# Optimization experiments

Measured on AMD Instinct MI355X. Metric: run time of the kernel, lower is better.

The kernel has to match this reference:

```python
import jax, jax.numpy as jnp
import numpy as np

COMPRESS_RATIO = 4
HEAD_DIM = 512
COFF = 2  # overlap (compress_ratio == 4) doubles the projection width
EPS = 1e-6


def setup_inputs() -> dict:
    key = jax.random.key(0)
    k1, k2, k3, k4 = jax.random.split(key, 4)
    B, S, D = 4, 4096, 4096
    OD = COFF * HEAD_DIM  # 1024
    scale = 1.0 / np.sqrt(D)
    return {
        "x": jax.random.normal(k1, (B, S, D), dtype=jnp.float32),
        "wkv_w": jax.random.normal(k2, (OD, D), dtype=jnp.float32) * scale,
        "wgate_w": jax.random.normal(k3, (OD, D), dtype=jnp.float32) * scale,
        "ape": jax.random.normal(k4, (COMPRESS_RATIO, OD), dtype=jnp.float32) * 0.02,
        "norm_w": jnp.ones((HEAD_DIM,), dtype=jnp.float32),
    }


def reference(x, wkv_w, wgate_w, ape, norm_w):
    # x: [B, S, D]; windowed KV compression (NSA-style):
    # gated projection -> per-position learned abs pos embed -> window pool -> RMSNorm
    B, S, D = x.shape
    r = COMPRESS_RATIO
    nW = S // r
    kv = jnp.einsum("bsd,od->bso", x, wkv_w)          # [B, S, coff*hd]
    gate = jax.nn.sigmoid(jnp.einsum("bsd,od->bso", x, wgate_w))
    kv = kv * gate
    # add learned absolute position embedding per position-within-window
    kv = kv + jnp.tile(ape, (nW, 1))                    # [S, coff*hd] broadcast over B
    # pool each window of r tokens; split overlap streams into separate tokens
    kv = kv.reshape(B, nW, r, COFF, HEAD_DIM).mean(axis=2)  # [B, nW, coff, hd]
    kv = kv.reshape(B, nW * COFF, HEAD_DIM)                 # [B, 2*nW, hd]
    # RMSNorm over head_dim
    var = jnp.mean(kv * kv, axis=-1, keepdims=True)
    return norm_w * kv * jax.lax.rsqrt(var + EPS)
```

## Files before the change

### kernel.cpp

```cpp
#include <hip/hip_runtime.h>
#include <hip/hip_bf16.h>

#define D_DIM 4096
#define OD    1024
#define M_TOT 16384
#define N_TOT 2048
#define BM 256
#define BN 256
#define BK 64

#define GLOBAL_AS __attribute__((address_space(1)))
#define LDS_AS    __attribute__((address_space(3)))

typedef __attribute__((ext_vector_type(8))) short          bf16x8;
typedef __attribute__((ext_vector_type(8))) unsigned short u16x8;
typedef __attribute__((ext_vector_type(4))) float          f32x4;

__device__ __forceinline__ unsigned short f2bf(float f) {
    unsigned int u = __float_as_uint(f);
    u = (u + 0x7fffu + ((u >> 16) & 1u)) >> 16;
    return (unsigned short)u;
}

__device__ __forceinline__ float sigm(float x) {
    return 1.0f / (1.0f + __expf(-x));
}

__device__ __forceinline__ void gload16(const void* g, void* l) {
    __builtin_amdgcn_global_load_lds((const GLOBAL_AS void*)g, (LDS_AS void*)l, 16, 0, 0);
}

__global__ void prep_weights(const float* __restrict__ wkv,
                             const float* __restrict__ wgate,
                             unsigned short* __restrict__ Wc) {
    int t  = blockIdx.x * 256 + threadIdx.x;
    int n  = t >> 9;
    int k8 = t & 511;
    const float* src = (n & 1) ? wgate : wkv;
    const float4* s4 = (const float4*)(src + (size_t)(n >> 1) * D_DIM + k8 * 8);
    float4 a = s4[0], b = s4[1];
    u16x8 o;
    o[0] = f2bf(a.x); o[1] = f2bf(a.y); o[2] = f2bf(a.z); o[3] = f2bf(a.w);
    o[4] = f2bf(b.x); o[5] = f2bf(b.y); o[6] = f2bf(b.z); o[7] = f2bf(b.w);
    *(u16x8*)(Wc + (size_t)n * D_DIM + k8 * 8) = o;
}

__global__ void prep_x(const float* __restrict__ x, unsigned short* __restrict__ xb) {
    size_t t = (size_t)blockIdx.x * 256 + threadIdx.x;
    const float4* s = (const float4*)(x + t * 8);
    float4 a = s[0], b = s[1];
    u16x8 o;
    o[0] = f2bf(a.x); o[1] = f2bf(a.y); o[2] = f2bf(a.z); o[3] = f2bf(a.w);
    o[4] = f2bf(b.x); o[5] = f2bf(b.y); o[6] = f2bf(b.z); o[7] = f2bf(b.w);
    *(u16x8*)(xb + t * 8) = o;
}

__global__ void prep_ape(const float* __restrict__ ape, float* __restrict__ am) {
    int t = blockIdx.x * 256 + threadIdx.x;
    if (t < OD)
        am[t] = 0.25f * (ape[t] + ape[OD + t] + ape[2 * OD + t] + ape[3 * OD + t]);
}

extern __shared__ __align__(16) unsigned short smem_u16[];

__global__ __launch_bounds__(512, 2)
void gemm_fused_8ph(const unsigned short* __restrict__ A,
                    const unsigned short* __restrict__ Wc,
                    const float* __restrict__ ape_mean,
                    float* __restrict__ out_pooled) {
    unsigned short* Asb[2] = {smem_u16,               smem_u16 + BM * BK};
    unsigned short* Bsb[2] = {smem_u16 + 2 * BM * BK, smem_u16 + 3 * BM * BK};

    const int tid  = threadIdx.x;
    const int lane = tid & 63;
    const int wave = tid >> 6;
    const int wm   = wave >> 2;
    const int wn   = wave & 3;
    const int h    = lane & 15;
    const int q    = lane >> 4;

    const int bid = blockIdx.x;
    const int j   = bid >> 3;
    const int m0  = ((bid & 7) * 8 + (j >> 3)) * BM;
    const int n0  = (j & 7) * BN;

    const int sc8 = (lane & 7) ^ ((lane >> 3) & 7);
    const unsigned short* Ag = A  + (size_t)(m0 + wave * 8 + (lane >> 3)) * D_DIM + sc8 * 8;
    const unsigned short* Bg = Wc + (size_t)(n0 + (wave & 3) * 8 + (lane >> 3)) * D_DIM + sc8 * 8;
    const int bstripe = wave >> 2;

#define STAGE_A(buf, half, kofs)                                                   \
    do {                                                                           \
        gload16(Ag + (size_t)((half) * 64) * D_DIM + (kofs),                       \
                Asb[buf] + ((half) * 64 + wave * 8) * BK);                         \
        gload16(Ag + (size_t)((half) * 64 + 128) * D_DIM + (kofs),                 \
                Asb[buf] + ((half) * 64 + 128 + wave * 8) * BK);                   \
    } while (0)

#define STAGE_B(buf, qb, kofs)                                                     \
    do {                                                                           \
        const int r0_ = (qb) * 32 + bstripe * 64;                                  \
        const int r1_ = (qb) * 32 + (2 + bstripe) * 64;                            \
        gload16(Bg + (size_t)r0_ * D_DIM + (kofs),                                 \
                Bsb[buf] + (r0_ + (wave & 3) * 8) * BK);                           \
        gload16(Bg + (size_t)r1_ * D_DIM + (kofs),                                 \
                Bsb[buf] + (r1_ + (wave & 3) * 8) * BK);                           \
    } while (0)

#define LOAD_A(buf, qa, dst)                                                       \
    do {                                                                           \
        _Pragma("unroll")                                                          \
        for (int mi = 0; mi < 4; ++mi) {                                           \
            const int row = wm * 128 + ((qa) * 4 + mi) * 16 + h;                   \
            _Pragma("unroll")                                                      \
            for (int ks = 0; ks < 2; ++ks)                                         \
                dst[mi][ks] = *(const bf16x8*)&Asb[buf][(row * BK + ks * 32 +      \
                              q * 8) ^ ((row & 7) << 3)];                          \
        }                                                                          \
    } while (0)

#define LOAD_B(buf, qb, dst)                                                       \
    do {                                                                           \
        _Pragma("unroll")                                                          \
        for (int ni = 0; ni < 2; ++ni) {                                           \
            const int rw = wn * 64 + ((qb) * 2 + ni) * 16 + h;                     \
            _Pragma("unroll")                                                      \
            for (int ks = 0; ks < 2; ++ks)                                         \
                dst[ni][ks] = *(const bf16x8*)&Bsb[buf][(rw * BK + ks * 32 +       \
                              q * 8) ^ ((rw & 7) << 3)];                           \
        }                                                                          \
    } while (0)

#define MFMA_Q(qa, qb, asrc, bsrc)                                                 \
    do {                                                                           \
        __builtin_amdgcn_s_setprio(1);                                             \
        _Pragma("unroll")                                                          \
        for (int mi = 0; mi < 4; ++mi)                                             \
            _Pragma("unroll")                                                      \
            for (int ni = 0; ni < 2; ++ni)                                         \
                _Pragma("unroll")                                                  \
                for (int ks = 0; ks < 2; ++ks)                                     \
                    acc[(qa) * 4 + mi][(qb) * 2 + ni] =                            \
                        __builtin_amdgcn_mfma_f32_16x16x32_bf16(                   \
                            asrc[mi][ks], bsrc[ni][ks],                            \
                            acc[(qa) * 4 + mi][(qb) * 2 + ni], 0, 0, 0);           \
        __builtin_amdgcn_s_setprio(0);                                             \
    } while (0)

#define BAR() __builtin_amdgcn_s_barrier()
#define VMW() asm volatile("s_waitcnt vmcnt(4)" ::: "memory")

    f32x4 acc[8][4];
    const f32x4 z = {0.f, 0.f, 0.f, 0.f};
#pragma unroll
    for (int i = 0; i < 8; ++i)
#pragma unroll
        for (int jj = 0; jj < 4; ++jj) acc[i][jj] = z;

    STAGE_A(0, 0, 0); STAGE_A(0, 1, 0); STAGE_B(0, 0, 0); STAGE_B(0, 1, 0);
    STAGE_B(1, 0, 64); STAGE_A(1, 0, 64);
    VMW();
    BAR();

    for (int kt2 = 0; kt2 < D_DIM; kt2 += 2 * BK) {
        const int kb1 = kt2 + BK;
        const int kna = (kt2 + 2 * BK) & 4095;
        const int knb = (kt2 + 3 * BK) & 4095;
        bf16x8 a_reg[4][2], b0r[2][2], b1r[2][2];

        LOAD_A(0, 0, a_reg); LOAD_B(0, 0, b0r);
        STAGE_A(1, 1, kb1);
        BAR(); MFMA_Q(0, 0, a_reg, b0r); BAR();
        LOAD_B(0, 1, b1r);
        STAGE_B(1, 1, kb1);
        BAR(); MFMA_Q(0, 1, a_reg, b1r); BAR();
        LOAD_A(0, 1, a_reg);
        STAGE_B(0, 0, kna);
        BAR(); MFMA_Q(1, 1, a_reg, b1r); BAR();
        STAGE_A(0, 0, kna);
        VMW();
        BAR(); MFMA_Q(1, 0, a_reg, b0r); BAR();

        LOAD_A(1, 0, a_reg); LOAD_B(1, 0, b0r);
        STAGE_A(0, 1, kna);
        BAR(); MFMA_Q(0, 0, a_reg, b0r); BAR();
        LOAD_B(1, 1, b1r);
        STAGE_B(0, 1, kna);
        BAR(); MFMA_Q(0, 1, a_reg, b1r); BAR();
        LOAD_A(1, 1, a_reg);
        STAGE_B(1, 0, knb);
        BAR(); MFMA_Q(1, 1, a_reg, b1r); BAR();
        STAGE_A(1, 0, knb);
        VMW();
        BAR(); MFMA_Q(1, 0, a_reg, b0r); BAR();
    }
#undef STAGE_A
#undef STAGE_B
#undef LOAD_A
#undef LOAD_B
#undef MFMA_Q
#undef BAR
#undef VMW

    const bool is_kv = ((h & 1) == 0);
#pragma unroll
    for (int mi = 0; mi < 8; ++mi) {
        const int mbase = m0 + wm * 128 + mi * 16 + q * 4;
        const int wglob = mbase >> 2;
#pragma unroll
        for (int ni = 0; ni < 4; ++ni) {
            f32x4 kv = acc[mi][ni];
            float g0 = __shfl_xor(kv[0], 1);
            float g1 = __shfl_xor(kv[1], 1);
            float g2 = __shfl_xor(kv[2], 1);
            float g3 = __shfl_xor(kv[3], 1);
            if (is_kv) {
                float s = kv[0] * sigm(g0) + kv[1] * sigm(g1) +
                          kv[2] * sigm(g2) + kv[3] * sigm(g3);
                int n = n0 + wn * 64 + ni * 16 + h;
                int o = n >> 1;
                out_pooled[(size_t)wglob * OD + o] = 0.25f * s + ape_mean[o];
            }
        }
    }
}

__global__ __launch_bounds__(256)
void gemm_fused_f32(const float* __restrict__ Aptr,
                    const unsigned short* __restrict__ Wc,
                    const float* __restrict__ ape_mean,
                    float* __restrict__ out_pooled) {
    __shared__ __align__(16) unsigned short As[128 * BK];
    __shared__ __align__(16) unsigned short Bs[128 * BK];
    const int tid  = threadIdx.x;
    const int lane = tid & 63;
    const int wave = tid >> 6;
    const int wr   = wave >> 1;
    const int wc   = wave & 1;
    const int n0   = blockIdx.x * 128;
    const int m0   = blockIdx.y * 128;
    const int h    = lane & 15;
    const int q    = lane >> 4;

    f32x4 acc[4][4];
    const f32x4 z = {0.f, 0.f, 0.f, 0.f};
#pragma unroll
    for (int i = 0; i < 4; ++i)
#pragma unroll
        for (int jj = 0; jj < 4; ++jj) acc[i][jj] = z;

    for (int kt = 0; kt < D_DIM; kt += BK) {
#pragma unroll
        for (int i = 0; i < 4; ++i) {
            int chunk = tid + i * 256;
            int row = chunk >> 3, c8 = chunk & 7;
            int dst = (row * BK + c8 * 8) ^ ((row & 7) << 3);
            const float4* s = (const float4*)(Aptr + (size_t)(m0 + row) * D_DIM + kt + c8 * 8);
            float4 a = s[0], b = s[1];
            u16x8 o;
            o[0] = f2bf(a.x); o[1] = f2bf(a.y); o[2] = f2bf(a.z); o[3] = f2bf(a.w);
            o[4] = f2bf(b.x); o[5] = f2bf(b.y); o[6] = f2bf(b.z); o[7] = f2bf(b.w);
            *(u16x8*)&As[dst] = o;
        }
#pragma unroll
        for (int i = 0; i < 4; ++i) {
            int chunk = tid + i * 256;
            int row = chunk >> 3, c8 = chunk & 7;
            int dst = (row * BK + c8 * 8) ^ ((row & 7) << 3);
            *(u16x8*)&Bs[dst] =
                *(const u16x8*)(Wc + (size_t)(n0 + row) * D_DIM + kt + c8 * 8);
        }
        __syncthreads();
#pragma unroll
        for (int ks = 0; ks < 2; ++ks) {
            const int kb = ks * 32 + q * 8;
            bf16x8 af[4], bfr[4];
#pragma unroll
            for (int am = 0; am < 4; ++am) {
                int row = wr * 64 + am * 16 + h;
                af[am] = *(const bf16x8*)&As[(row * BK + kb) ^ ((row & 7) << 3)];
            }
#pragma unroll
            for (int bn = 0; bn < 4; ++bn) {
                int row = wc * 64 + bn * 16 + h;
                bfr[bn] = *(const bf16x8*)&Bs[(row * BK + kb) ^ ((row & 7) << 3)];
            }
#pragma unroll
            for (int am = 0; am < 4; ++am)
#pragma unroll
                for (int bn = 0; bn < 4; ++bn)
                    acc[am][bn] = __builtin_amdgcn_mfma_f32_16x16x32_bf16(
                        af[am], bfr[bn], acc[am][bn], 0, 0, 0);
        }
        __syncthreads();
    }
    const bool is_kv = ((h & 1) == 0);
#pragma unroll
    for (int am = 0; am < 4; ++am) {
        const int mbase = m0 + wr * 64 + am * 16 + q * 4;
        const int wglob = mbase >> 2;
#pragma unroll
        for (int bn = 0; bn < 4; ++bn) {
            f32x4 kv = acc[am][bn];
            float g0 = __shfl_xor(kv[0], 1);
            float g1 = __shfl_xor(kv[1], 1);
            float g2 = __shfl_xor(kv[2], 1);
            float g3 = __shfl_xor(kv[3], 1);
            if (is_kv) {
                float s = kv[0] * sigm(g0) + kv[1] * sigm(g1) +
                          kv[2] * sigm(g2) + kv[3] * sigm(g3);
                int n = n0 + wc * 64 + bn * 16 + h;
                int o = n >> 1;
                out_pooled[(size_t)wglob * OD + o] = 0.25f * s + ape_mean[o];
            }
        }
    }
}

__global__ void rmsnorm_inplace(float* __restrict__ out, const float* __restrict__ nw) {
    int token = blockIdx.x * 4 + (threadIdx.x >> 6);
    int lane  = threadIdx.x & 63;
    float4* p = (float4*)(out + (size_t)token * 512);
    float4 v0 = p[lane * 2], v1 = p[lane * 2 + 1];
    float ss = v0.x * v0.x + v0.y * v0.y + v0.z * v0.z + v0.w * v0.w +
               v1.x * v1.x + v1.y * v1.y + v1.z * v1.z + v1.w * v1.w;
#pragma unroll
    for (int off = 32; off > 0; off >>= 1) ss += __shfl_xor(ss, off);
    float rs = rsqrtf(ss * (1.0f / 512.0f) + 1e-6f);
    const float4* w4 = (const float4*)nw;
    float4 w0 = w4[lane * 2], w1 = w4[lane * 2 + 1];
    float4 r0, r1;
    r0.x = v0.x * rs * w0.x; r0.y = v0.y * rs * w0.y;
    r0.z = v0.z * rs * w0.z; r0.w = v0.w * rs * w0.w;
    r1.x = v1.x * rs * w1.x; r1.y = v1.y * rs * w1.y;
    r1.z = v1.z * rs * w1.z; r1.w = v1.w * rs * w1.w;
    p[lane * 2]     = r0;
    p[lane * 2 + 1] = r1;
}

extern "C" void kernel_launch(void* const* d_in, const int* in_sizes, int n_in,
                              void* d_out, int out_size, void* d_ws, size_t ws_size,
                              hipStream_t stream) {
    const float* x     = (const float*)d_in[0];
    const float* wkv   = (const float*)d_in[1];
    const float* wgate = (const float*)d_in[2];
    const float* ape   = (const float*)d_in[3];
    const float* normw = (const float*)d_in[4];
    float* out = (float*)d_out;

    unsigned short* Wc  = (unsigned short*)d_ws;
    float* ape_mean     = (float*)((char*)d_ws + (size_t)16 * 1024 * 1024);
    unsigned short* xb  = (unsigned short*)((char*)d_ws + (size_t)16 * 1024 * 1024 + 65536);
    const size_t need_xb = (size_t)16 * 1024 * 1024 + 65536 + (size_t)M_TOT * D_DIM * 2;
    const bool use_xb = (ws_size >= need_xb);

    prep_weights<<<4096, 256, 0, stream>>>(wkv, wgate, Wc);
    prep_ape<<<4, 256, 0, stream>>>(ape, ape_mean);

    if (use_xb) {
        prep_x<<<32768, 256, 0, stream>>>(x, xb);
        (void)hipFuncSetAttribute(
            reinterpret_cast<const void*>(&gemm_fused_8ph),
            hipFuncAttributeMaxDynamicSharedMemorySize, 131072);
        gemm_fused_8ph<<<(M_TOT / BM) * (N_TOT / BN), 512, 131072, stream>>>(
            xb, Wc, ape_mean, out);
    } else {
        gemm_fused_f32<<<dim3(N_TOT / 128, M_TOT / 128), 256, 0, stream>>>(
            x, Wc, ape_mean, out);
    }

    rmsnorm_inplace<<<2048, 256, 0, stream>>>(out, normw);
}
```

Measured before the change: 373.5 us.

## Reorder GEMM quadrant schedule to reuse single A/B register set and deepen prefetch

Restructures the ping-pong main loop so that only one A and one B fragment buffer live in registers, visiting the quadrants in a zig-zag order (00,10,11,01) and reloading A for the last quadrant. Prefetch staging is shifted one step earlier, so three tiles are in flight at the prologue and vmcnt waits at 6 instead of 4. This aims to cut register pressure and leave more global loads outstanding, at the cost of an extra LDS read of A per half-iteration.

```diff
diff --git a/kernel.cpp b/kernel.cpp
--- a/kernel.cpp
+++ b/kernel.cpp
@@ -148,7 +148,7 @@
     } while (0)
 
 #define BAR() __builtin_amdgcn_s_barrier()
-#define VMW() asm volatile("s_waitcnt vmcnt(4)" ::: "memory")
+#define VMW6() asm volatile("s_waitcnt vmcnt(6)" ::: "memory")
 
     f32x4 acc[8][4];
     const f32x4 z = {0.f, 0.f, 0.f, 0.f};
@@ -158,41 +158,43 @@
         for (int jj = 0; jj < 4; ++jj) acc[i][jj] = z;
 
     STAGE_A(0, 0, 0); STAGE_A(0, 1, 0); STAGE_B(0, 0, 0); STAGE_B(0, 1, 0);
-    STAGE_B(1, 0, 64); STAGE_A(1, 0, 64);
-    VMW();
+    STAGE_B(1, 0, 64); STAGE_A(1, 1, 64); STAGE_B(1, 1, 64);
+    VMW6();
     BAR();
 
     for (int kt2 = 0; kt2 < D_DIM; kt2 += 2 * BK) {
         const int kb1 = kt2 + BK;
         const int kna = (kt2 + 2 * BK) & 4095;
         const int knb = (kt2 + 3 * BK) & 4095;
-        bf16x8 a_reg[4][2], b0r[2][2], b1r[2][2];
-
-        LOAD_A(0, 0, a_reg); LOAD_B(0, 0, b0r);
-        STAGE_A(1, 1, kb1);
-        BAR(); MFMA_Q(0, 0, a_reg, b0r); BAR();
-        LOAD_B(0, 1, b1r);
-        STAGE_B(1, 1, kb1);
-        BAR(); MFMA_Q(0, 1, a_reg, b1r); BAR();
-        LOAD_A(0, 1, a_reg);
+        bf16x8 av[4][2], bv[2][2];
+
+        LOAD_A(0, 0, av); LOAD_B(0, 0, bv);
+        STAGE_A(1, 0, kb1);
+        BAR(); MFMA_Q(0, 0, av, bv); BAR();
+        LOAD_A(0, 1, av);
         STAGE_B(0, 0, kna);
-        BAR(); MFMA_Q(1, 1, a_reg, b1r); BAR();
+        BAR(); MFMA_Q(1, 0, av, bv); BAR();
+        LOAD_B(0, 1, bv);
+        STAGE_A(0, 1, kna);
+        BAR(); MFMA_Q(1, 1, av, bv); BAR();
+        LOAD_A(0, 0, av);
+        STAGE_B(0, 1, kna);
+        VMW6();
+        BAR(); MFMA_Q(0, 1, av, bv); BAR();
+
+        LOAD_A(1, 0, av); LOAD_B(1, 0, bv);
         STAGE_A(0, 0, kna);
-        VMW();
-        BAR(); MFMA_Q(1, 0, a_reg, b0r); BAR();
-
-        LOAD_A(1, 0, a_reg); LOAD_B(1, 0, b0r);
-        STAGE_A(0, 1, kna);
-        BAR(); MFMA_Q(0, 0, a_reg, b0r); BAR();
-        LOAD_B(1, 1, b1r);
-        STAGE_B(0, 1, kna);
-        BAR(); MFMA_Q(0, 1, a_reg, b1r); BAR();
-        LOAD_A(1, 1, a_reg);
+        BAR(); MFMA_Q(0, 0, av, bv); BAR();
+        LOAD_A(1, 1, av);
         STAGE_B(1, 0, knb);
-        BAR(); MFMA_Q(1, 1, a_reg, b1r); BAR();
-        STAGE_A(1, 0, knb);
-        VMW();
-        BAR(); MFMA_Q(1, 0, a_reg, b0r); BAR();
+        BAR(); MFMA_Q(1, 0, av, bv); BAR();
+        LOAD_B(1, 1, bv);
+        STAGE_A(1, 1, knb);
+        BAR(); MFMA_Q(1, 1, av, bv); BAR();
+        LOAD_A(1, 0, av);
+        STAGE_B(1, 1, knb);
+        VMW6();
+        BAR(); MFMA_Q(0, 1, av, bv); BAR();
     }
 #undef STAGE_A
 #undef STAGE_B
@@ -200,7 +202,7 @@
 #undef LOAD_B
 #undef MFMA_Q
 #undef BAR
-#undef VMW
+#undef VMW6
 
     const bool is_kv = ((h & 1) == 0);
 #pragma unroll
```

Result: faster. 311.3 us (-16.7%).
